# Kernel tuning notes

Measured on AMD Instinct MI355X. Metric: run time of the kernel, lower is better.

The kernel has to match this reference:

```python
import jax, jax.numpy as jnp
import numpy as np

N_NODES = 100000
N_EDGES = 600000
HID = 128
CH_OUT = 3


def setup_inputs() -> dict:
    key = jax.random.key(0)
    ks = jax.random.split(key, 16)
    s = 0.05  # small init to keep tanh in its linear-ish range
    inp = {
        "x": jax.random.normal(ks[0], (N_NODES, HID), dtype=jnp.float32),
        "pos": jax.random.normal(ks[1], (N_NODES, 3), dtype=jnp.float32),
        "edge_index": jax.random.randint(ks[2], (2, N_EDGES), 0, N_NODES, dtype=jnp.int32),
        "fe_w1": jax.random.normal(ks[3], (2 * HID + 1, HID), dtype=jnp.float32) * s,
        "fe_b1": jnp.zeros((HID,), jnp.float32),
        "fe_w2": jax.random.normal(ks[4], (HID, HID), dtype=jnp.float32) * s,
        "fe_b2": jnp.zeros((HID,), jnp.float32),
        "finf_w": jax.random.normal(ks[5], (HID, 1), dtype=jnp.float32) * s,
        "finf_b": jnp.zeros((1,), jnp.float32),
        "fh_w1": jax.random.normal(ks[6], (2 * HID, HID), dtype=jnp.float32) * s,
        "fh_b1": jnp.zeros((HID,), jnp.float32),
        "fh_w2": jax.random.normal(ks[7], (HID, HID), dtype=jnp.float32) * s,
        "fh_b2": jnp.zeros((HID,), jnp.float32),
        "l1_w": jax.random.normal(ks[8], (HID, HID), dtype=jnp.float32) * s,
        "l1_b": jnp.zeros((HID,), jnp.float32),
        "l2_w": jax.random.normal(ks[9], (HID, HID), dtype=jnp.float32) * s,
        "l2_b": jnp.zeros((HID,), jnp.float32),
        "l3_w": jax.random.normal(ks[10], (HID, HID), dtype=jnp.float32) * s,
        "l3_b": jnp.zeros((HID,), jnp.float32),
        "l4_w": jax.random.normal(ks[11], (HID, HID), dtype=jnp.float32) * s,
        "l4_b": jnp.zeros((HID,), jnp.float32),
        "l5_w": jax.random.normal(ks[12], (HID, CH_OUT), dtype=jnp.float32) * s,
        "l5_b": jnp.zeros((CH_OUT,), jnp.float32),
    }
    return inp


def reference(x, pos, edge_index, fe_w1, fe_b1, fe_w2, fe_b2, finf_w, finf_b,
              fh_w1, fh_b1, fh_w2, fh_b2, l1_w, l1_b, l2_w, l2_b, l3_w, l3_b,
              l4_w, l4_b, l5_w, l5_b):
    e_st, e_end = edge_index[0], edge_index[1]
    # dists = ||(pos_i - pos_j)^2||_2  (norm of the squared difference, as in source)
    d = pos[e_st] - pos[e_end]                                  # [E, 3]
    dists = jnp.linalg.norm(jnp.square(d), axis=1, keepdims=True)  # [E, 1]
    # edge MLP f_e
    tmp = jnp.concatenate([x[e_st], x[e_end], dists], axis=1)   # [E, 2H+1]
    m_ij = jnp.tanh(tmp @ fe_w1 + fe_b1)
    m_ij = jnp.tanh(m_ij @ fe_w2 + fe_b2)                        # [E, H]
    # gating f_inf
    e_ij = jnp.tanh(m_ij @ finf_w + finf_b)                      # [E, 1]
    # scatter-sum to source nodes (index_add on edge_index[0])
    m_i = jax.ops.segment_sum(e_ij * m_ij, e_st, num_segments=x.shape[0])  # [N, H]
    # node update f_h with residual
    h = jnp.concatenate([x, m_i], axis=1)                        # [N, 2H]
    x = x + (jnp.tanh(h @ fh_w1 + fh_b1) @ fh_w2 + fh_b2)
    # dense head (dropout p=0.0 is identity)
    lrelu = lambda v: jax.nn.leaky_relu(v, negative_slope=0.01)
    x = lrelu(x @ l1_w + l1_b)
    x = lrelu(x @ l2_w + l2_b)
    x = lrelu(x @ l3_w + l3_b)
    x = lrelu(x @ l4_w + l4_b)
    return x @ l5_w + l5_b
```

## Files before the change

### kernel.cpp

```cpp
#include <hip/hip_runtime.h>
#include <math.h>

#define HID 128

typedef unsigned short u16;
typedef __attribute__((ext_vector_type(8))) short bfrag;
typedef __attribute__((ext_vector_type(4))) float f32x4;
typedef __attribute__((ext_vector_type(8))) unsigned short u16x8;
typedef __attribute__((ext_vector_type(4))) unsigned short u16x4;

__device__ __forceinline__ float fast_tanh(float v) {
    v = fminf(15.0f, fmaxf(-15.0f, v));
    float e = __expf(2.0f * v);
    float r = __builtin_amdgcn_rcpf(e + 1.0f);
    return 1.0f - 2.0f * r;
}

__device__ __forceinline__ u16 f2b(float f) {
    union { float f; unsigned int u; } v;
    v.f = f;
    unsigned int u = v.u;
    return (u16)((u + 0x7FFFu + ((u >> 16) & 1u)) >> 16);
}
__device__ __forceinline__ float b2f(u16 b) {
    union { unsigned int u; float f; } v;
    v.u = ((unsigned int)b) << 16;
    return v.f;
}
__device__ __forceinline__ float bits2f(unsigned u) {
    union { unsigned u; float f; } v; v.u = u; return v.f;
}

__global__ void __launch_bounds__(256) prep_x(const float* __restrict__ x,
                                              u16* __restrict__ xb) {
    int i = blockIdx.x * 256 + threadIdx.x;
    const float4 v0 = *(const float4*)(x + (size_t)i * 8);
    const float4 v1 = *(const float4*)(x + (size_t)i * 8 + 4);
    u16x8 o = { f2b(v0.x), f2b(v0.y), f2b(v0.z), f2b(v0.w),
                f2b(v1.x), f2b(v1.y), f2b(v1.z), f2b(v1.w) };
    *(u16x8*)(xb + (size_t)i * 8) = o;
}

__global__ void __launch_bounds__(256) prep_weights(
    const float* __restrict__ w1, const float* __restrict__ fh1,
    const float* __restrict__ w2, const float* __restrict__ fh2,
    const float* __restrict__ l1, const float* __restrict__ l2,
    const float* __restrict__ l3, const float* __restrict__ l4,
    u16* __restrict__ w1t, u16* __restrict__ fh1t,
    u16* __restrict__ w2t, u16* __restrict__ fh2t,
    u16* __restrict__ l1t, u16* __restrict__ l2t,
    u16* __restrict__ l3t, u16* __restrict__ l4t)
{
    int b = blockIdx.x, t = threadIdx.x;
    const float* src; u16* dst; int K;
    if (b < 256) {
        K = 256;
        if (b < 128) { src = w1;  dst = w1t; }
        else         { src = fh1; dst = fh1t; b -= 128; }
    } else {
        K = 128;
        int s = (b - 256) >> 6; b = (b - 256) & 63;
        switch (s) {
            case 0:  src = w2;  dst = w2t;  break;
            case 1:  src = fh2; dst = fh2t; break;
            case 2:  src = l1;  dst = l1t;  break;
            case 3:  src = l2;  dst = l2t;  break;
            case 4:  src = l3;  dst = l3t;  break;
            default: src = l4;  dst = l4t;  break;
        }
    }
    int idx = b * 256 + t;
    int k = idx >> 7, n = idx & 127;
    dst[(size_t)n * K + k] = f2b(src[(size_t)k * 128 + n]);
}

__global__ void __launch_bounds__(256) hist_kernel(const int* __restrict__ est,
                                                   int* __restrict__ cnt, int E) {
    int e = blockIdx.x * 256 + threadIdx.x;
    if (e < E) atomicAdd(&cnt[est[e]], 1);
}

__global__ void __launch_bounds__(256) scan1(const int* __restrict__ cnt,
                                             int* __restrict__ scanout,
                                             int* __restrict__ partial, int N) {
    __shared__ int s[256];
    int t = threadIdx.x, b = blockIdx.x, i = b * 256 + t;
    int v = (i < N) ? cnt[i] : 0;
    s[t] = v; __syncthreads();
#pragma unroll
    for (int d = 1; d < 256; d <<= 1) {
        int add = (t >= d) ? s[t - d] : 0;
        __syncthreads();
        s[t] += add;
        __syncthreads();
    }
    if (i < N) scanout[i] = s[t] - v;
    if (t == 255) partial[b] = s[255];
}

__global__ void __launch_bounds__(512) scan2(int* __restrict__ partial, int NB) {
    __shared__ int s[512];
    int t = threadIdx.x;
    int v = (t < NB) ? partial[t] : 0;
    s[t] = v; __syncthreads();
#pragma unroll
    for (int d = 1; d < 512; d <<= 1) {
        int add = (t >= d) ? s[t - d] : 0;
        __syncthreads();
        s[t] += add;
        __syncthreads();
    }
    if (t < NB) partial[t] = s[t] - v;
}

__global__ void __launch_bounds__(256) scan3(const int* __restrict__ scanout,
                                             const int* __restrict__ partial,
                                             int* __restrict__ offs,
                                             int* __restrict__ cur, int N, int E) {
    int t = threadIdx.x, b = blockIdx.x, i = b * 256 + t;
    if (i < N) { int o = scanout[i] + partial[b]; offs[i] = o; cur[i] = o; }
    if (i == 0) offs[N] = E;
}

__global__ void __launch_bounds__(256) reorder_kernel(const int* __restrict__ est,
                                                      int* __restrict__ cur,
                                                      int* __restrict__ inv, int E) {
    int e = blockIdx.x * 256 + threadIdx.x;
    if (e < E) { int p = atomicAdd(&cur[est[e]], 1); inv[e] = p; }
}

template<int KD>
__device__ __forceinline__ void gemm_k(const u16* sbuf, const u16* __restrict__ wt,
                                       int w, int l16, int l4g, f32x4 (&acc)[2][2]) {
    const int RS = KD * 2;
#pragma unroll
    for (int k0 = 0; k0 < KD; k0 += 32) {
        const int kb = k0 * 2 + l4g * 16;
        bfrag a0 = *(const bfrag*)((const char*)sbuf +
                    (unsigned)((l16 * RS + kb) ^ ((l16 & 7) << 4)));
        bfrag a1 = *(const bfrag*)((const char*)sbuf +
                    (unsigned)(((16 + l16) * RS + kb) ^ ((l16 & 7) << 4)));
        bfrag b0 = *(const bfrag*)((const char*)wt + (size_t)(32 * w + l16) * RS + kb);
        bfrag b1 = *(const bfrag*)((const char*)wt + (size_t)(32 * w + 16 + l16) * RS + kb);
        acc[0][0] = __builtin_amdgcn_mfma_f32_16x16x32_bf16(a0, b0, acc[0][0], 0, 0, 0);
        acc[0][1] = __builtin_amdgcn_mfma_f32_16x16x32_bf16(a0, b1, acc[0][1], 0, 0, 0);
        acc[1][0] = __builtin_amdgcn_mfma_f32_16x16x32_bf16(a1, b0, acc[1][0], 0, 0, 0);
        acc[1][1] = __builtin_amdgcn_mfma_f32_16x16x32_bf16(a1, b1, acc[1][1], 0, 0, 0);
    }
}

__global__ void __launch_bounds__(256, 2)
egc_edge_csr(const u16* __restrict__ xb, const float* __restrict__ pos,
             const int* __restrict__ est, const int* __restrict__ eend,
             const int* __restrict__ inv,
             const u16* __restrict__ w1t, const float* __restrict__ w1last,
             const float* __restrict__ b1, const u16* __restrict__ w2t,
             const float* __restrict__ b2, u16* __restrict__ g, int n_tiles)
{
    __shared__ __attribute__((aligned(16))) u16 a_sh[2][32 * 256];
    __shared__ __attribute__((aligned(16))) u16 m1_sh[32 * 128];
    __shared__ float dist_l[2][32];
    __shared__ int   dst_l[2][32];

    const int t = threadIdx.x, lane = t & 63, w = t >> 6;
    const int l16 = lane & 15, l4g = lane >> 4;
    const unsigned swz = (unsigned)((l16 & 7) << 4);

    bfrag wa10[8], wa11[8], w2f0[4], w2f1[4];
#pragma unroll
    for (int i = 0; i < 8; ++i) {
        int kb = i * 64 + l4g * 16;
        wa10[i] = *(const bfrag*)((const char*)w1t + (size_t)(32 * w + l16) * 512 + kb);
        wa11[i] = *(const bfrag*)((const char*)w1t + (size_t)(32 * w + 16 + l16) * 512 + kb);
    }
#pragma unroll
    for (int i = 0; i < 4; ++i) {
        int kb = i * 64 + l4g * 16;
        w2f0[i] = *(const bfrag*)((const char*)w2t + (size_t)(32 * w + l16) * 256 + kb);
        w2f1[i] = *(const bfrag*)((const char*)w2t + (size_t)(32 * w + 16 + l16) * 256 + kb);
    }
    float w1l_r[2][4], b1_r[2][4], b2_r[2][4];
#pragma unroll
    for (int mi = 0; mi < 2; ++mi)
#pragma unroll
        for (int rg = 0; rg < 4; ++rg) {
            int n = 32 * w + 16 * mi + l4g * 4 + rg;
            w1l_r[mi][rg] = w1last[n];
            b1_r[mi][rg]  = b1[n];
            b2_r[mi][rg]  = b2[n];
        }

    float4 sv0, sv1, sv2, sv3;
    float pax = 0, pay = 0, paz = 0, pbx = 0, pby = 0, pbz = 0;
    int sdst = 0;

#define EDGE_ISSUE(TILE) do {                                                  \
        int e0_ = (TILE) * 32;                                                 \
        { int f_ = t;       int e_ = f_ >> 5, q_ = f_ & 31; int ge_ = e0_ + e_;\
          int nd_ = (q_ < 16) ? est[ge_] : eend[ge_];                          \
          sv0 = *(const float4*)(xb + (size_t)nd_ * 128 + (q_ & 15) * 8); }    \
        { int f_ = t + 256; int e_ = f_ >> 5, q_ = f_ & 31; int ge_ = e0_ + e_;\
          int nd_ = (q_ < 16) ? est[ge_] : eend[ge_];                          \
          sv1 = *(const float4*)(xb + (size_t)nd_ * 128 + (q_ & 15) * 8); }    \
        { int f_ = t + 512; int e_ = f_ >> 5, q_ = f_ & 31; int ge_ = e0_ + e_;\
          int nd_ = (q_ < 16) ? est[ge_] : eend[ge_];                          \
          sv2 = *(const float4*)(xb + (size_t)nd_ * 128 + (q_ & 15) * 8); }    \
        { int f_ = t + 768; int e_ = f_ >> 5, q_ = f_ & 31; int ge_ = e0_ + e_;\
          int nd_ = (q_ < 16) ? est[ge_] : eend[ge_];                          \
          sv3 = *(const float4*)(xb + (size_t)nd_ * 128 + (q_ & 15) * 8); }    \
        if (t < 32) {                                                          \
            int ge_ = e0_ + t;                                                 \
            int a_ = est[ge_], b_ = eend[ge_];                                 \
            sdst = inv[ge_];                                                   \
            pax = pos[a_ * 3]; pay = pos[a_ * 3 + 1]; paz = pos[a_ * 3 + 2];   \
            pbx = pos[b_ * 3]; pby = pos[b_ * 3 + 1]; pbz = pos[b_ * 3 + 2];   \
        }                                                                      \
    } while (0)

#define EDGE_COMMIT(BUF) do {                                                  \
        { int f_ = t;       int e_ = f_ >> 5, q_ = f_ & 31;                    \
          unsigned by_ = (unsigned)(e_ * 512 + q_ * 16) ^ (unsigned)((e_ & 7) << 4); \
          *(float4*)((char*)a_sh[BUF] + by_) = sv0; }                          \
        { int f_ = t + 256; int e_ = f_ >> 5, q_ = f_ & 31;                    \
          unsigned by_ = (unsigned)(e_ * 512 + q_ * 16) ^ (unsigned)((e_ & 7) << 4); \
          *(float4*)((char*)a_sh[BUF] + by_) = sv1; }                          \
        { int f_ = t + 512; int e_ = f_ >> 5, q_ = f_ & 31;                    \
          unsigned by_ = (unsigned)(e_ * 512 + q_ * 16) ^ (unsigned)((e_ & 7) << 4); \
          *(float4*)((char*)a_sh[BUF] + by_) = sv2; }                          \
        { int f_ = t + 768; int e_ = f_ >> 5, q_ = f_ & 31;                    \
          unsigned by_ = (unsigned)(e_ * 512 + q_ * 16) ^ (unsigned)((e_ & 7) << 4); \
          *(float4*)((char*)a_sh[BUF] + by_) = sv3; }                          \
        if (t < 32) {                                                          \
            float dx_ = pax - pbx, dy_ = pay - pby, dz_ = paz - pbz;           \
            dx_ *= dx_; dy_ *= dy_; dz_ *= dz_;                                \
            dist_l[BUF][t] = sqrtf(dx_ * dx_ + dy_ * dy_ + dz_ * dz_);         \
            dst_l[BUF][t] = sdst;                                              \
        }                                                                      \
    } while (0)

    int tile = blockIdx.x;
    EDGE_ISSUE(tile);
    int buf = 0;

    while (true) {
        EDGE_COMMIT(buf);
        __syncthreads();
        int next = tile + gridDim.x;
        if (next < n_tiles) EDGE_ISSUE(next);

        {
            f32x4 acc[2][2] = {};
#pragma unroll
            for (int i = 0; i < 8; ++i) {
                int kb = i * 64 + l4g * 16;
                bfrag be0 = *(const bfrag*)((const char*)a_sh[buf] +
                            ((unsigned)(l16 * 512 + kb) ^ swz));
                bfrag be1 = *(const bfrag*)((const char*)a_sh[buf] +
                            ((unsigned)((16 + l16) * 512 + kb) ^ swz));
                acc[0][0] = __builtin_amdgcn_mfma_f32_16x16x32_bf16(wa10[i], be0, acc[0][0], 0, 0, 0);
                acc[0][1] = __builtin_amdgcn_mfma_f32_16x16x32_bf16(wa10[i], be1, acc[0][1], 0, 0, 0);
                acc[1][0] = __builtin_amdgcn_mfma_f32_16x16x32_bf16(wa11[i], be0, acc[1][0], 0, 0, 0);
                acc[1][1] = __builtin_amdgcn_mfma_f32_16x16x32_bf16(wa11[i], be1, acc[1][1], 0, 0, 0);
            }
            float de0 = dist_l[buf][l16];
            float de1 = dist_l[buf][16 + l16];
#pragma unroll
            for (int mi = 0; mi < 2; ++mi)
#pragma unroll
                for (int ni = 0; ni < 2; ++ni) {
                    float de = ni ? de1 : de0;
                    u16x4 pk;
#pragma unroll
                    for (int rg = 0; rg < 4; ++rg) {
                        float v = fast_tanh(acc[mi][ni][rg] + de * w1l_r[mi][rg] + b1_r[mi][rg]);
                        pk[rg] = f2b(v);
                    }
                    unsigned byte = ((unsigned)((16 * ni + l16) * 256 +
                                     (32 * w + 16 * mi + l4g * 4) * 2)) ^ swz;
                    *(u16x4*)((char*)m1_sh + byte) = pk;
                }
        }
        __syncthreads();

        {
            f32x4 acc[2][2] = {};
#pragma unroll
            for (int i = 0; i < 4; ++i) {
                int kb = i * 64 + l4g * 16;
                bfrag me0 = *(const bfrag*)((const char*)m1_sh +
                            ((unsigned)(l16 * 256 + kb) ^ swz));
                bfrag me1 = *(const bfrag*)((const char*)m1_sh +
                            ((unsigned)((16 + l16) * 256 + kb) ^ swz));
                acc[0][0] = __builtin_amdgcn_mfma_f32_16x16x32_bf16(w2f0[i], me0, acc[0][0], 0, 0, 0);
                acc[0][1] = __builtin_amdgcn_mfma_f32_16x16x32_bf16(w2f0[i], me1, acc[0][1], 0, 0, 0);
                acc[1][0] = __builtin_amdgcn_mfma_f32_16x16x32_bf16(w2f1[i], me0, acc[1][0], 0, 0, 0);
                acc[1][1] = __builtin_amdgcn_mfma_f32_16x16x32_bf16(w2f1[i], me1, acc[1][1], 0, 0, 0);
            }
            int dr0 = dst_l[buf][l16];
            int dr1 = dst_l[buf][16 + l16];
#pragma unroll
            for (int mi = 0; mi < 2; ++mi)
#pragma unroll
                for (int ni = 0; ni < 2; ++ni) {
                    u16x4 pk;
#pragma unroll
                    for (int rg = 0; rg < 4; ++rg)
                        pk[rg] = f2b(fast_tanh(acc[mi][ni][rg] + b2_r[mi][rg]));
                    int dstrow = ni ? dr1 : dr0;
                    u16* dp = g + (size_t)dstrow * 128 + (32 * w + 16 * mi + l4g * 4);
                    *(u16x4*)dp = pk;
                }
        }

        tile = next; buf ^= 1;
        if (tile >= n_tiles) break;
    }
#undef EDGE_ISSUE
#undef EDGE_COMMIT
}

__global__ void __launch_bounds__(256, 8)
gather_gate(const u16* __restrict__ g, const int* __restrict__ offs,
            const float* __restrict__ fw, const float* __restrict__ fb,
            u16* __restrict__ m_i)
{
    const int lane = threadIdx.x & 63;
    const int n = blockIdx.x * 4 + (threadIdx.x >> 6);
    const float fw0 = fw[2 * lane], fw1 = fw[2 * lane + 1];
    const float fbv = fb[0];
    const int beg = offs[n], end = offs[n + 1];
    const unsigned* g32 = (const unsigned*)g;
    float a0 = 0.0f, a1 = 0.0f;
    int e = beg;
    for (; e + 1 < end; e += 2) {
        unsigned v0 = g32[(size_t)e * 64 + lane];
        unsigned v1 = g32[(size_t)(e + 1) * 64 + lane];
        float f00 = bits2f(v0 << 16), f01 = bits2f(v0 & 0xFFFF0000u);
        float f10 = bits2f(v1 << 16), f11 = bits2f(v1 & 0xFFFF0000u);
        float s0 = f00 * fw0 + f01 * fw1;
        float s1 = f10 * fw0 + f11 * fw1;
#pragma unroll
        for (int m = 1; m < 64; m <<= 1) {
            s0 += __shfl_xor(s0, m);
            s1 += __shfl_xor(s1, m);
        }
        float ev0 = fast_tanh(s0 + fbv);
        float ev1 = fast_tanh(s1 + fbv);
        a0 += ev0 * f00 + ev1 * f10;
        a1 += ev0 * f01 + ev1 * f11;
    }
    if (e < end) {
        unsigned v0 = g32[(size_t)e * 64 + lane];
        float f00 = bits2f(v0 << 16), f01 = bits2f(v0 & 0xFFFF0000u);
        float s0 = f00 * fw0 + f01 * fw1;
#pragma unroll
        for (int m = 1; m < 64; m <<= 1) s0 += __shfl_xor(s0, m);
        float ev0 = fast_tanh(s0 + fbv);
        a0 += ev0 * f00;
        a1 += ev0 * f01;
    }
    unsigned o = (unsigned)f2b(a0) | ((unsigned)f2b(a1) << 16);
    ((unsigned*)m_i)[(size_t)n * 64 + lane] = o;
}

__global__ void __launch_bounds__(256, 3)
egc_edge_mfma(const u16* __restrict__ xb, const float* __restrict__ pos,
              const int* __restrict__ est, const int* __restrict__ eend,
              const u16* __restrict__ w1t, const float* __restrict__ w1last,
              const float* __restrict__ b1, const u16* __restrict__ w2t,
              const float* __restrict__ b2, const float* __restrict__ fw,
              const float* __restrict__ fb, float* __restrict__ m_i)
{
    __shared__ __attribute__((aligned(16))) u16 a_sh[32 * 256];
    __shared__ __attribute__((aligned(16))) u16 m1_sh[32 * 128];
    __shared__ float m2_sh[32][132];
    __shared__ float dist_l[32];
    __shared__ float ev_l[32];
    __shared__ int   st_l[32];

    const int t = threadIdx.x;
    const int e0 = blockIdx.x * 32;
    const int lane = t & 63;
    const int w = t >> 6;
    const int l16 = lane & 15, l4g = lane >> 4;

#pragma unroll
    for (int i = 0; i < 4; ++i) {
        int f = t + 256 * i;
        int e = f >> 5, q = f & 31;
        int ge = e0 + e;
        int node = (q < 16) ? est[ge] : eend[ge];
        float4 v = *(const float4*)(xb + (size_t)node * 128 + (q & 15) * 8);
        unsigned byte = (unsigned)(e * 512 + q * 16) ^ (unsigned)((e & 7) << 4);
        *(float4*)((char*)a_sh + byte) = v;
    }
    if (t < 32) {
        int ge = e0 + t;
        int a = est[ge], b = eend[ge];
        st_l[t] = a;
        float dx = pos[a * 3 + 0] - pos[b * 3 + 0];
        float dy = pos[a * 3 + 1] - pos[b * 3 + 1];
        float dz = pos[a * 3 + 2] - pos[b * 3 + 2];
        dx *= dx; dy *= dy; dz *= dz;
        dist_l[t] = sqrtf(dx * dx + dy * dy + dz * dz);
    }
    __syncthreads();

    {
        f32x4 acc[2][2] = {};
        gemm_k<256>(a_sh, w1t, w, l16, l4g, acc);
#pragma unroll
        for (int mi = 0; mi < 2; ++mi)
#pragma unroll
            for (int ni = 0; ni < 2; ++ni) {
                const int col = 32 * w + 16 * ni + l16;
                const float wl = w1last[col], bb = b1[col];
#pragma unroll
                for (int rg = 0; rg < 4; ++rg) {
                    const int row = 16 * mi + l4g * 4 + rg;
                    float v = fast_tanh(acc[mi][ni][rg] + dist_l[row] * wl + bb);
                    unsigned byte = (unsigned)((row * 256 + col * 2) ^ ((row & 7) << 4));
                    *(u16*)((char*)m1_sh + byte) = f2b(v);
                }
            }
    }
    __syncthreads();

    {
        f32x4 acc[2][2] = {};
        gemm_k<128>(m1_sh, w2t, w, l16, l4g, acc);
#pragma unroll
        for (int mi = 0; mi < 2; ++mi)
#pragma unroll
            for (int ni = 0; ni < 2; ++ni) {
                const int col = 32 * w + 16 * ni + l16;
                const float bb = b2[col];
#pragma unroll
                for (int rg = 0; rg < 4; ++rg) {
                    const int row = 16 * mi + l4g * 4 + rg;
                    m2_sh[row][col] = fast_tanh(acc[mi][ni][rg] + bb);
                }
            }
    }
    __syncthreads();

    if (t < 128) {
        int e = t >> 2, p = t & 3;
        float s = 0.0f;
#pragma unroll
        for (int k = 0; k < 32; ++k) s += m2_sh[e][p * 32 + k] * fw[p * 32 + k];
        s += __shfl_xor(s, 1);
        s += __shfl_xor(s, 2);
        if (p == 0) ev_l[e] = fast_tanh(s + fb[0]);
    }
    __syncthreads();

    {
        int e = t >> 3, l8 = t & 7;
        float ev = ev_l[e];
        size_t base = (size_t)st_l[e] * HID + l8;
#pragma unroll
        for (int i = 0; i < 16; ++i)
            unsafeAtomicAdd(m_i + base + 8 * i, ev * m2_sh[e][l8 + 8 * i]);
    }
}

#define NODE_LAYER(SRC, KD, WT, BIAS, EPILOG)                                  \
    {                                                                          \
        f32x4 acc[2][2] = {};                                                  \
        gemm_k<KD>(SRC, WT, w, l16, l4g, acc);                                 \
        _Pragma("unroll")                                                      \
        for (int mi = 0; mi < 2; ++mi)                                         \
            _Pragma("unroll")                                                  \
            for (int ni = 0; ni < 2; ++ni) {                                   \
                const int col = 32 * w + 16 * ni + l16;                        \
                const float bb = (BIAS)[col];                                  \
                _Pragma("unroll")                                              \
                for (int rg = 0; rg < 4; ++rg) {                               \
                    const int row = 16 * mi + l4g * 4 + rg;                    \
                    float v = acc[mi][ni][rg] + bb;                            \
                    EPILOG;                                                    \
                }                                                              \
            }                                                                  \
    }

#define STORE_BF16(DST) do {                                                   \
        unsigned byte = (unsigned)((row * 256 + col * 2) ^ ((row & 7) << 4));  \
        *(u16*)((char*)(DST) + byte) = f2b(v);                                 \
    } while (0)

template<bool MIBF16>
__global__ void __launch_bounds__(256, 3)
egc_node_mfma(const u16* __restrict__ xb, const float* __restrict__ xf,
              const void* __restrict__ m_i,
              const u16* __restrict__ fh1t, const float* __restrict__ hb1,
              const u16* __restrict__ fh2t, const float* __restrict__ hb2,
              const u16* __restrict__ l1t, const float* __restrict__ l1b,
              const u16* __restrict__ l2t, const float* __restrict__ l2b,
              const u16* __restrict__ l3t, const float* __restrict__ l3b,
              const u16* __restrict__ l4t, const float* __restrict__ l4b,
              const float* __restrict__ l5w, const float* __restrict__ l5b,
              float* __restrict__ out)
{
    __shared__ __attribute__((aligned(16))) u16 a_sh[32 * 256];
    __shared__ __attribute__((aligned(16))) u16 bA[32 * 128];
    __shared__ __attribute__((aligned(16))) u16 bB[32 * 128];
    __shared__ float ff[32][132];

    const int t = threadIdx.x;
    const int n0 = blockIdx.x * 32;
    const int lane = t & 63;
    const int w = t >> 6;
    const int l16 = lane & 15, l4g = lane >> 4;

#pragma unroll
    for (int i = 0; i < 2; ++i) {
        int f = t + 256 * i;
        int n = f >> 4, q = f & 15;
        float4 v = *(const float4*)(xb + (size_t)(n0 + n) * 128 + q * 8);
        unsigned byte = (unsigned)((n * 512 + q * 16) ^ ((n & 7) << 4));
        *(float4*)((char*)a_sh + byte) = v;
    }
    if (MIBF16) {
#pragma unroll
        for (int i = 0; i < 2; ++i) {
            int f = t + 256 * i;
            int n = f >> 4, q = f & 15;
            float4 v = *(const float4*)((const u16*)m_i + (size_t)(n0 + n) * 128 + q * 8);
            unsigned byte = (unsigned)((n * 512 + 256 + q * 16) ^ ((n & 7) << 4));
            *(float4*)((char*)a_sh + byte) = v;
        }
    } else {
#pragma unroll
        for (int i = 0; i < 2; ++i) {
            int f = t + 256 * i;
            int n = f >> 4, q = f & 15;
            const float* src = (const float*)m_i + (size_t)(n0 + n) * 128 + q * 8;
            float4 v0 = *(const float4*)(src);
            float4 v1 = *(const float4*)(src + 4);
            u16x8 o = { f2b(v0.x), f2b(v0.y), f2b(v0.z), f2b(v0.w),
                        f2b(v1.x), f2b(v1.y), f2b(v1.z), f2b(v1.w) };
            unsigned byte = (unsigned)((n * 512 + 256 + q * 16) ^ ((n & 7) << 4));
            *(u16x8*)((char*)a_sh + byte) = o;
        }
    }
    __syncthreads();

    NODE_LAYER(a_sh, 256, fh1t, hb1, { v = fast_tanh(v); STORE_BF16(bA); })
    __syncthreads();
    NODE_LAYER(bA, 128, fh2t, hb2,
               { v += xf[(size_t)(n0 + row) * HID + col]; STORE_BF16(bB); })
    __syncthreads();
    NODE_LAYER(bB, 128, l1t, l1b, { v = v > 0.0f ? v : 0.01f * v; STORE_BF16(bA); })
    __syncthreads();
    NODE_LAYER(bA, 128, l2t, l2b, { v = v > 0.0f ? v : 0.01f * v; STORE_BF16(bB); })
    __syncthreads();
    NODE_LAYER(bB, 128, l3t, l3b, { v = v > 0.0f ? v : 0.01f * v; STORE_BF16(bA); })
    __syncthreads();
    NODE_LAYER(bA, 128, l4t, l4b, { ff[row][col] = v > 0.0f ? v : 0.01f * v; })
    __syncthreads();

    if (t < 96) {
        int n = t / 3, cc = t % 3;
        float s = l5b[cc];
#pragma unroll 8
        for (int k = 0; k < HID; ++k) s += ff[n][k] * l5w[k * 3 + cc];
        out[(size_t)(n0 + n) * 3 + cc] = s;
    }
}

extern "C" void kernel_launch(void* const* d_in, const int* in_sizes, int n_in,
                              void* d_out, int out_size, void* d_ws, size_t ws_size,
                              hipStream_t stream)
{
    const float* x      = (const float*)d_in[0];
    const float* pos    = (const float*)d_in[1];
    const int*   eidx   = (const int*)d_in[2];
    const float* fe_w1  = (const float*)d_in[3];
    const float* fe_b1  = (const float*)d_in[4];
    const float* fe_w2  = (const float*)d_in[5];
    const float* fe_b2  = (const float*)d_in[6];
    const float* finf_w = (const float*)d_in[7];
    const float* finf_b = (const float*)d_in[8];
    const float* fh_w1  = (const float*)d_in[9];
    const float* fh_b1  = (const float*)d_in[10];
    const float* fh_w2  = (const float*)d_in[11];
    const float* fh_b2  = (const float*)d_in[12];
    const float* l1w    = (const float*)d_in[13];
    const float* l1b    = (const float*)d_in[14];
    const float* l2w    = (const float*)d_in[15];
    const float* l2b    = (const float*)d_in[16];
    const float* l3w    = (const float*)d_in[17];
    const float* l3b    = (const float*)d_in[18];
    const float* l4w    = (const float*)d_in[19];
    const float* l4b    = (const float*)d_in[20];
    const float* l5w    = (const float*)d_in[21];
    const float* l5b    = (const float*)d_in[22];
    float* out = (float*)d_out;

    const int n_edges = in_sizes[2] / 2;
    const int n_nodes = in_sizes[0] / HID;
    const int nsb     = (n_nodes + 255) / 256;
    const int n_tiles = n_edges / 32;

    char* ws = (char*)d_ws;
    const bool use_csr = (ws_size >= 208800000ULL);

    if (use_csr) {
        u16* g    = (u16*)(ws + 0);
        u16* xb   = (u16*)(ws + 153600000);
        u16* m_i  = (u16*)(ws + 179200000);
        u16* w1t  = (u16*)(ws + 204800000);
        u16* w2t  = (u16*)(ws + 204865536);
        u16* fh1t = (u16*)(ws + 204898304);
        u16* fh2t = (u16*)(ws + 204963840);
        u16* l1t  = (u16*)(ws + 204996608);
        u16* l2t  = (u16*)(ws + 205029376);
        u16* l3t  = (u16*)(ws + 205062144);
        u16* l4t  = (u16*)(ws + 205094912);
        int* cnt  = (int*)(ws + 205127680);
        int* offs = (int*)(ws + 205527680);
        int* cur  = (int*)(ws + 205927696);
        int* inv  = (int*)(ws + 206327696);
        int* part = (int*)(ws + 208727696);

        (void)hipMemsetAsync(cnt, 0, (size_t)n_nodes * sizeof(int), stream);
        prep_x<<<dim3((n_nodes * HID) / (256 * 8)), dim3(256), 0, stream>>>(x, xb);
        prep_weights<<<dim3(640), dim3(256), 0, stream>>>(
            fe_w1, fh_w1, fe_w2, fh_w2, l1w, l2w, l3w, l4w,
            w1t, fh1t, w2t, fh2t, l1t, l2t, l3t, l4t);

        hist_kernel<<<dim3((n_edges + 255) / 256), dim3(256), 0, stream>>>(eidx, cnt, n_edges);
        scan1<<<dim3(nsb), dim3(256), 0, stream>>>(cnt, cnt, part, n_nodes);
        scan2<<<dim3(1), dim3(512), 0, stream>>>(part, nsb);
        scan3<<<dim3(nsb), dim3(256), 0, stream>>>(cnt, part, offs, cur, n_nodes, n_edges);
        reorder_kernel<<<dim3((n_edges + 255) / 256), dim3(256), 0, stream>>>(eidx, cur, inv, n_edges);

        egc_edge_csr<<<dim3(512), dim3(256), 0, stream>>>(
            xb, pos, eidx, eidx + n_edges, inv, w1t, fe_w1 + (size_t)256 * HID, fe_b1,
            w2t, fe_b2, g, n_tiles);

        gather_gate<<<dim3(n_nodes / 4), dim3(256), 0, stream>>>(g, offs, finf_w, finf_b, m_i);

        egc_node_mfma<true><<<dim3(n_nodes / 32), dim3(256), 0, stream>>>(
            xb, x, m_i, fh1t, fh_b1, fh2t, fh_b2, l1t, l1b, l2t, l2b,
            l3t, l3b, l4t, l4b, l5w, l5b, out);
    } else {
        float* m_i = (float*)(ws + 0);
        u16* xb    = (u16*)(ws + 51200000);
        u16* w1t   = (u16*)(ws + 76800000);
        u16* w2t   = (u16*)(ws + 76865536);
        u16* fh1t  = (u16*)(ws + 76898304);
        u16* fh2t  = (u16*)(ws + 76963840);
        u16* l1t   = (u16*)(ws + 76996608);
        u16* l2t   = (u16*)(ws + 77029376);
        u16* l3t   = (u16*)(ws + 77062144);
        u16* l4t   = (u16*)(ws + 77094912);

        (void)hipMemsetAsync(m_i, 0, (size_t)n_nodes * HID * sizeof(float), stream);
        prep_x<<<dim3((n_nodes * HID) / (256 * 8)), dim3(256), 0, stream>>>(x, xb);
        prep_weights<<<dim3(640), dim3(256), 0, stream>>>(
            fe_w1, fh_w1, fe_w2, fh_w2, l1w, l2w, l3w, l4w,
            w1t, fh1t, w2t, fh2t, l1t, l2t, l3t, l4t);

        egc_edge_mfma<<<dim3(n_edges / 32), dim3(256), 0, stream>>>(
            xb, pos, eidx, eidx + n_edges, w1t, fe_w1 + (size_t)256 * HID, fe_b1,
            w2t, fe_b2, finf_w, finf_b, m_i);

        egc_node_mfma<false><<<dim3(n_nodes / 32), dim3(256), 0, stream>>>(
            xb, x, m_i, fh1t, fh_b1, fh2t, fh_b2, l1t, l1b, l2t, l2b,
            l3t, l3b, l4t, l4b, l5w, l5b, out);
    }
}
```

Before: 384.3 us.

## Sort edges by source, fuse gate into edge kernel, swap node GEMM operands

The reorder kernel now writes sorted source/destination index arrays, so the edge kernel processes edges in CSR order and writes g rows sequentially instead of scattering through an inverse permutation. The f_inf gate dot product and tanh move into the edge kernel epilogue, computed once per edge via a shared-memory reduction. The gather then becomes a plain weighted sum without per-edge wave shuffles. The node kernel swaps the MFMA operands so each lane stores four contiguous channels as vector stores instead of scalar bf16 stores. Occupancy hint and edge grid size also rise. Costs are an extra __syncthreads per tile and est_s/eend_s aliasing the m_i buffer, which is safe only because m_i is written after the edge kernel finishes.

```diff
diff --git a/kernel.cpp b/kernel.cpp
--- a/kernel.cpp
+++ b/kernel.cpp
@@ -123,10 +123,17 @@
 }
 
 __global__ void __launch_bounds__(256) reorder_kernel(const int* __restrict__ est,
+                                                      const int* __restrict__ eend,
                                                       int* __restrict__ cur,
-                                                      int* __restrict__ inv, int E) {
+                                                      int* __restrict__ est_s,
+                                                      int* __restrict__ eend_s, int E) {
     int e = blockIdx.x * 256 + threadIdx.x;
-    if (e < E) { int p = atomicAdd(&cur[est[e]], 1); inv[e] = p; }
+    if (e < E) {
+        int s = est[e];
+        int p = atomicAdd(&cur[s], 1);
+        est_s[p]  = s;
+        eend_s[p] = eend[e];
+    }
 }
 
 template<int KD>
@@ -149,18 +156,39 @@
     }
 }
 
-__global__ void __launch_bounds__(256, 2)
+template<int KD>
+__device__ __forceinline__ void gemm_sw(const u16* act, const u16* __restrict__ wt,
+                                        int w, int l16, int l4g, f32x4 (&acc)[2][2]) {
+    const int RS = KD * 2;
+#pragma unroll
+    for (int k0 = 0; k0 < KD; k0 += 32) {
+        const int kb = k0 * 2 + l4g * 16;
+        bfrag wa0 = *(const bfrag*)((const char*)wt + (size_t)(32 * w + l16) * RS + kb);
+        bfrag wa1 = *(const bfrag*)((const char*)wt + (size_t)(32 * w + 16 + l16) * RS + kb);
+        bfrag be0 = *(const bfrag*)((const char*)act +
+                    (unsigned)((l16 * RS + kb) ^ ((l16 & 7) << 4)));
+        bfrag be1 = *(const bfrag*)((const char*)act +
+                    (unsigned)(((16 + l16) * RS + kb) ^ ((l16 & 7) << 4)));
+        acc[0][0] = __builtin_amdgcn_mfma_f32_16x16x32_bf16(wa0, be0, acc[0][0], 0, 0, 0);
+        acc[0][1] = __builtin_amdgcn_mfma_f32_16x16x32_bf16(wa0, be1, acc[0][1], 0, 0, 0);
+        acc[1][0] = __builtin_amdgcn_mfma_f32_16x16x32_bf16(wa1, be0, acc[1][0], 0, 0, 0);
+        acc[1][1] = __builtin_amdgcn_mfma_f32_16x16x32_bf16(wa1, be1, acc[1][1], 0, 0, 0);
+    }
+}
+
+__global__ void __launch_bounds__(256, 3)
 egc_edge_csr(const u16* __restrict__ xb, const float* __restrict__ pos,
-             const int* __restrict__ est, const int* __restrict__ eend,
-             const int* __restrict__ inv,
+             const int* __restrict__ est_s, const int* __restrict__ eend_s,
              const u16* __restrict__ w1t, const float* __restrict__ w1last,
              const float* __restrict__ b1, const u16* __restrict__ w2t,
-             const float* __restrict__ b2, u16* __restrict__ g, int n_tiles)
+             const float* __restrict__ b2, const float* __restrict__ fw,
+             const float* __restrict__ fb, u16* __restrict__ g,
+             float* __restrict__ ev, int n_tiles)
 {
     __shared__ __attribute__((aligned(16))) u16 a_sh[2][32 * 256];
     __shared__ __attribute__((aligned(16))) u16 m1_sh[32 * 128];
+    __shared__ float red[32][16];
     __shared__ float dist_l[2][32];
-    __shared__ int   dst_l[2][32];
 
     const int t = threadIdx.x, lane = t & 63, w = t >> 6;
     const int l16 = lane & 15, l4g = lane >> 4;
@@ -179,7 +207,7 @@
         w2f0[i] = *(const bfrag*)((const char*)w2t + (size_t)(32 * w + l16) * 256 + kb);
         w2f1[i] = *(const bfrag*)((const char*)w2t + (size_t)(32 * w + 16 + l16) * 256 + kb);
     }
-    float w1l_r[2][4], b1_r[2][4], b2_r[2][4];
+    float w1l_r[2][4], b1_r[2][4], b2_r[2][4], fw_r[2][4];
 #pragma unroll
     for (int mi = 0; mi < 2; ++mi)
 #pragma unroll
@@ -188,30 +216,30 @@
             w1l_r[mi][rg] = w1last[n];
             b1_r[mi][rg]  = b1[n];
             b2_r[mi][rg]  = b2[n];
+            fw_r[mi][rg]  = fw[n];
         }
+    const float fbv = fb[0];
 
     float4 sv0, sv1, sv2, sv3;
     float pax = 0, pay = 0, paz = 0, pbx = 0, pby = 0, pbz = 0;
-    int sdst = 0;
 
 #define EDGE_ISSUE(TILE) do {                                                  \
         int e0_ = (TILE) * 32;                                                 \
         { int f_ = t;       int e_ = f_ >> 5, q_ = f_ & 31; int ge_ = e0_ + e_;\
-          int nd_ = (q_ < 16) ? est[ge_] : eend[ge_];                          \
+          int nd_ = (q_ < 16) ? est_s[ge_] : eend_s[ge_];                      \
           sv0 = *(const float4*)(xb + (size_t)nd_ * 128 + (q_ & 15) * 8); }    \
         { int f_ = t + 256; int e_ = f_ >> 5, q_ = f_ & 31; int ge_ = e0_ + e_;\
-          int nd_ = (q_ < 16) ? est[ge_] : eend[ge_];                          \
+          int nd_ = (q_ < 16) ? est_s[ge_] : eend_s[ge_];                      \
           sv1 = *(const float4*)(xb + (size_t)nd_ * 128 + (q_ & 15) * 8); }    \
         { int f_ = t + 512; int e_ = f_ >> 5, q_ = f_ & 31; int ge_ = e0_ + e_;\
-          int nd_ = (q_ < 16) ? est[ge_] : eend[ge_];                          \
+          int nd_ = (q_ < 16) ? est_s[ge_] : eend_s[ge_];                      \
           sv2 = *(const float4*)(xb + (size_t)nd_ * 128 + (q_ & 15) * 8); }    \
         { int f_ = t + 768; int e_ = f_ >> 5, q_ = f_ & 31; int ge_ = e0_ + e_;\
-          int nd_ = (q_ < 16) ? est[ge_] : eend[ge_];                          \
+          int nd_ = (q_ < 16) ? est_s[ge_] : eend_s[ge_];                      \
           sv3 = *(const float4*)(xb + (size_t)nd_ * 128 + (q_ & 15) * 8); }    \
         if (t < 32) {                                                          \
             int ge_ = e0_ + t;                                                 \
-            int a_ = est[ge_], b_ = eend[ge_];                                 \
-            sdst = inv[ge_];                                                   \
+            int a_ = est_s[ge_], b_ = eend_s[ge_];                             \
             pax = pos[a_ * 3]; pay = pos[a_ * 3 + 1]; paz = pos[a_ * 3 + 2];   \
             pbx = pos[b_ * 3]; pby = pos[b_ * 3 + 1]; pbz = pos[b_ * 3 + 2];   \
         }                                                                      \
@@ -234,7 +262,6 @@
             float dx_ = pax - pbx, dy_ = pay - pby, dz_ = paz - pbz;           \
             dx_ *= dx_; dy_ *= dy_; dz_ *= dz_;                                \
             dist_l[BUF][t] = sqrtf(dx_ * dx_ + dy_ * dy_ + dz_ * dz_);         \
-            dst_l[BUF][t] = sdst;                                              \
         }                                                                      \
     } while (0)
 
@@ -247,6 +274,7 @@
         __syncthreads();
         int next = tile + gridDim.x;
         if (next < n_tiles) EDGE_ISSUE(next);
+        const int e0 = tile * 32;
 
         {
             f32x4 acc[2][2] = {};
@@ -296,20 +324,33 @@
                 acc[1][0] = __builtin_amdgcn_mfma_f32_16x16x32_bf16(w2f1[i], me0, acc[1][0], 0, 0, 0);
                 acc[1][1] = __builtin_amdgcn_mfma_f32_16x16x32_bf16(w2f1[i], me1, acc[1][1], 0, 0, 0);
             }
-            int dr0 = dst_l[buf][l16];
-            int dr1 = dst_l[buf][16 + l16];
+            float part0 = 0.0f, part1 = 0.0f;
 #pragma unroll
             for (int mi = 0; mi < 2; ++mi)
 #pragma unroll
                 for (int ni = 0; ni < 2; ++ni) {
                     u16x4 pk;
-#pragma unroll
-                    for (int rg = 0; rg < 4; ++rg)
-                        pk[rg] = f2b(fast_tanh(acc[mi][ni][rg] + b2_r[mi][rg]));
-                    int dstrow = ni ? dr1 : dr0;
-                    u16* dp = g + (size_t)dstrow * 128 + (32 * w + 16 * mi + l4g * 4);
-                    *(u16x4*)dp = pk;
+                    float ps = 0.0f;
+#pragma unroll
+                    for (int rg = 0; rg < 4; ++rg) {
+                        float v = fast_tanh(acc[mi][ni][rg] + b2_r[mi][rg]);
+                        ps += v * fw_r[mi][rg];
+                        pk[rg] = f2b(v);
+                    }
+                    if (ni) part1 += ps; else part0 += ps;
+                    int dstrow = e0 + 16 * ni + l16;
+                    *(u16x4*)(g + (size_t)dstrow * 128 + (32 * w + 16 * mi + l4g * 4)) = pk;
                 }
+            red[l16][w * 4 + l4g]      = part0;
+            red[16 + l16][w * 4 + l4g] = part1;
+        }
+        __syncthreads();
+
+        if (t < 32) {
+            float s = 0.0f;
+#pragma unroll
+            for (int j = 0; j < 16; ++j) s += red[t][j];
+            ev[e0 + t] = fast_tanh(s + fbv);
         }
 
         tile = next; buf ^= 1;
@@ -320,45 +361,31 @@
 }
 
 __global__ void __launch_bounds__(256, 8)
-gather_gate(const u16* __restrict__ g, const int* __restrict__ offs,
-            const float* __restrict__ fw, const float* __restrict__ fb,
-            u16* __restrict__ m_i)
+gather_seq(const u16* __restrict__ g, const float* __restrict__ ev,
+           const int* __restrict__ offs, u16* __restrict__ m_i)
 {
     const int lane = threadIdx.x & 63;
     const int n = blockIdx.x * 4 + (threadIdx.x >> 6);
-    const float fw0 = fw[2 * lane], fw1 = fw[2 * lane + 1];
-    const float fbv = fb[0];
     const int beg = offs[n], end = offs[n + 1];
     const unsigned* g32 = (const unsigned*)g;
-    float a0 = 0.0f, a1 = 0.0f;
+    float a0 = 0.0f, a1 = 0.0f, b0 = 0.0f, b1 = 0.0f;
     int e = beg;
     for (; e + 1 < end; e += 2) {
         unsigned v0 = g32[(size_t)e * 64 + lane];
         unsigned v1 = g32[(size_t)(e + 1) * 64 + lane];
-        float f00 = bits2f(v0 << 16), f01 = bits2f(v0 & 0xFFFF0000u);
-        float f10 = bits2f(v1 << 16), f11 = bits2f(v1 & 0xFFFF0000u);
-        float s0 = f00 * fw0 + f01 * fw1;
-        float s1 = f10 * fw0 + f11 * fw1;
-#pragma unroll
-        for (int m = 1; m < 64; m <<= 1) {
-            s0 += __shfl_xor(s0, m);
-            s1 += __shfl_xor(s1, m);
-        }
-        float ev0 = fast_tanh(s0 + fbv);
-        float ev1 = fast_tanh(s1 + fbv);
-        a0 += ev0 * f00 + ev1 * f10;
-        a1 += ev0 * f01 + ev1 * f11;
+        float e0 = ev[e], e1 = ev[e + 1];
+        a0 += e0 * bits2f(v0 << 16);
+        a1 += e0 * bits2f(v0 & 0xFFFF0000u);
+        b0 += e1 * bits2f(v1 << 16);
+        b1 += e1 * bits2f(v1 & 0xFFFF0000u);
     }
     if (e < end) {
         unsigned v0 = g32[(size_t)e * 64 + lane];
-        float f00 = bits2f(v0 << 16), f01 = bits2f(v0 & 0xFFFF0000u);
-        float s0 = f00 * fw0 + f01 * fw1;
-#pragma unroll
-        for (int m = 1; m < 64; m <<= 1) s0 += __shfl_xor(s0, m);
-        float ev0 = fast_tanh(s0 + fbv);
-        a0 += ev0 * f00;
-        a1 += ev0 * f01;
-    }
+        float e0 = ev[e];
+        a0 += e0 * bits2f(v0 << 16);
+        a1 += e0 * bits2f(v0 & 0xFFFF0000u);
+    }
+    a0 += b0; a1 += b1;
     unsigned o = (unsigned)f2b(a0) | ((unsigned)f2b(a1) << 16);
     ((unsigned*)m_i)[(size_t)n * 64 + lane] = o;
 }
@@ -465,29 +492,33 @@
     }
 }
 
-#define NODE_LAYER(SRC, KD, WT, BIAS, EPILOG)                                  \
+#define NODE_LAYER_SW(SRC, KD, WT, BIAS, DST, ACT)                             \
     {                                                                          \
         f32x4 acc[2][2] = {};                                                  \
-        gemm_k<KD>(SRC, WT, w, l16, l4g, acc);                                 \
+        gemm_sw<KD>(SRC, WT, w, l16, l4g, acc);                                \
+        float bbr[2][4];                                                       \
+        _Pragma("unroll")                                                      \
+        for (int mi = 0; mi < 2; ++mi)                                         \
+            _Pragma("unroll")                                                  \
+            for (int rg = 0; rg < 4; ++rg)                                     \
+                bbr[mi][rg] = (BIAS)[32 * w + 16 * mi + l4g * 4 + rg];         \
         _Pragma("unroll")                                                      \
         for (int mi = 0; mi < 2; ++mi)                                         \
             _Pragma("unroll")                                                  \
             for (int ni = 0; ni < 2; ++ni) {                                   \
-                const int col = 32 * w + 16 * ni + l16;                        \
-                const float bb = (BIAS)[col];                                  \
+                const int node = 16 * ni + l16;                                \
+                const int ch = 32 * w + 16 * mi + l4g * 4;                     \
+                u16x4 pk;                                                      \
                 _Pragma("unroll")                                              \
                 for (int rg = 0; rg < 4; ++rg) {                               \
-                    const int row = 16 * mi + l4g * 4 + rg;                    \
-                    float v = acc[mi][ni][rg] + bb;                            \
-                    EPILOG;                                                    \
+                    float v = acc[mi][ni][rg] + bbr[mi][rg];                   \
+                    ACT;                                                       \
+                    pk[rg] = f2b(v);                                           \
                 }                                                              \
+                unsigned byte = ((unsigned)(node * 256 + ch * 2)) ^ swz;       \
+                *(u16x4*)((char*)(DST) + byte) = pk;                           \
             }                                                                  \
     }
-
-#define STORE_BF16(DST) do {                                                   \
-        unsigned byte = (unsigned)((row * 256 + col * 2) ^ ((row & 7) << 4));  \
-        *(u16*)((char*)(DST) + byte) = f2b(v);                                 \
-    } while (0)
 
 template<bool MIBF16>
 __global__ void __launch_bounds__(256, 3)
@@ -512,6 +543,7 @@
     const int lane = t & 63;
     const int w = t >> 6;
     const int l16 = lane & 15, l4g = lane >> 4;
+    const unsigned swz = (unsigned)((l16 & 7) << 4);
 
 #pragma unroll
     for (int i = 0; i < 2; ++i) {
@@ -546,18 +578,70 @@
     }
     __syncthreads();
 
-    NODE_LAYER(a_sh, 256, fh1t, hb1, { v = fast_tanh(v); STORE_BF16(bA); })
-    __syncthreads();
-    NODE_LAYER(bA, 128, fh2t, hb2,
-               { v += xf[(size_t)(n0 + row) * HID + col]; STORE_BF16(bB); })
-    __syncthreads();
-    NODE_LAYER(bB, 128, l1t, l1b, { v = v > 0.0f ? v : 0.01f * v; STORE_BF16(bA); })
-    __syncthreads();
-    NODE_LAYER(bA, 128, l2t, l2b, { v = v > 0.0f ? v : 0.01f * v; STORE_BF16(bB); })
-    __syncthreads();
-    NODE_LAYER(bB, 128, l3t, l3b, { v = v > 0.0f ? v : 0.01f * v; STORE_BF16(bA); })
-    __syncthreads();
-    NODE_LAYER(bA, 128, l4t, l4b, { ff[row][col] = v > 0.0f ? v : 0.01f * v; })
+    NODE_LAYER_SW(a_sh, 256, fh1t, hb1, bA, { v = fast_tanh(v); })
+    __syncthreads();
+
+    {
+        f32x4 acc[2][2] = {};
+        gemm_sw<128>(bA, fh2t, w, l16, l4g, acc);
+        float bbr[2][4];
+#pragma unroll
+        for (int mi = 0; mi < 2; ++mi)
+#pragma unroll
+            for (int rg = 0; rg < 4; ++rg)
+                bbr[mi][rg] = hb2[32 * w + 16 * mi + l4g * 4 + rg];
+#pragma unroll
+        for (int mi = 0; mi < 2; ++mi)
+#pragma unroll
+            for (int ni = 0; ni < 2; ++ni) {
+                const int node = 16 * ni + l16;
+                const int ch = 32 * w + 16 * mi + l4g * 4;
+                float4 xr = *(const float4*)(xf + (size_t)(n0 + node) * 128 + ch);
+                u16x4 pk;
+                pk[0] = f2b(acc[mi][ni][0] + bbr[mi][0] + xr.x);
+                pk[1] = f2b(acc[mi][ni][1] + bbr[mi][1] + xr.y);
+                pk[2] = f2b(acc[mi][ni][2] + bbr[mi][2] + xr.z);
+                pk[3] = f2b(acc[mi][ni][3] + bbr[mi][3] + xr.w);
+                unsigned byte = ((unsigned)(node * 256 + ch * 2)) ^ swz;
+                *(u16x4*)((char*)bB + byte) = pk;
+            }
+    }
+    __syncthreads();
+
+    NODE_LAYER_SW(bB, 128, l1t, l1b, bA, { v = v > 0.0f ? v : 0.01f * v; })
+    __syncthreads();
+    NODE_LAYER_SW(bA, 128, l2t, l2b, bB, { v = v > 0.0f ? v : 0.01f * v; })
+    __syncthreads();
+    NODE_LAYER_SW(bB, 128, l3t, l3b, bA, { v = v > 0.0f ? v : 0.01f * v; })
+    __syncthreads();
+
+    {
+        f32x4 acc[2][2] = {};
+        gemm_sw<128>(bA, l4t, w, l16, l4g, acc);
+        float bbr[2][4];
+#pragma unroll
+        for (int mi = 0; mi < 2; ++mi)
+#pragma unroll
+            for (int rg = 0; rg < 4; ++rg)
+                bbr[mi][rg] = l4b[32 * w + 16 * mi + l4g * 4 + rg];
+#pragma unroll
+        for (int mi = 0; mi < 2; ++mi)
+#pragma unroll
+            for (int ni = 0; ni < 2; ++ni) {
+                const int node = 16 * ni + l16;
+                const int ch = 32 * w + 16 * mi + l4g * 4;
+                float4 o;
+                float v0 = acc[mi][ni][0] + bbr[mi][0];
+                float v1 = acc[mi][ni][1] + bbr[mi][1];
+                float v2 = acc[mi][ni][2] + bbr[mi][2];
+                float v3 = acc[mi][ni][3] + bbr[mi][3];
+                o.x = v0 > 0.0f ? v0 : 0.01f * v0;
+                o.y = v1 > 0.0f ? v1 : 0.01f * v1;
+                o.z = v2 > 0.0f ? v2 : 0.01f * v2;
+                o.w = v3 > 0.0f ? v3 : 0.01f * v3;
+                *(float4*)(&ff[node][ch]) = o;
+            }
+    }
     __syncthreads();
 
     if (t < 96) {
@@ -607,9 +691,11 @@
     const bool use_csr = (ws_size >= 208800000ULL);
 
     if (use_csr) {
-        u16* g    = (u16*)(ws + 0);
-        u16* xb   = (u16*)(ws + 153600000);
-        u16* m_i  = (u16*)(ws + 179200000);
+        u16* g     = (u16*)(ws + 0);
+        u16* xb    = (u16*)(ws + 153600000);
+        u16* m_i   = (u16*)(ws + 179200000);
+        int* est_s  = (int*)(ws + 179200000);
+        int* eend_s = (int*)(ws + 181600000);
         u16* w1t  = (u16*)(ws + 204800000);
         u16* w2t  = (u16*)(ws + 204865536);
         u16* fh1t = (u16*)(ws + 204898304);
@@ -621,7 +707,7 @@
         int* cnt  = (int*)(ws + 205127680);
         int* offs = (int*)(ws + 205527680);
         int* cur  = (int*)(ws + 205927696);
-        int* inv  = (int*)(ws + 206327696);
+        float* ev = (float*)(ws + 206327696);
         int* part = (int*)(ws + 208727696);
 
         (void)hipMemsetAsync(cnt, 0, (size_t)n_nodes * sizeof(int), stream);
@@ -634,13 +720,14 @@
         scan1<<<dim3(nsb), dim3(256), 0, stream>>>(cnt, cnt, part, n_nodes);
         scan2<<<dim3(1), dim3(512), 0, stream>>>(part, nsb);
         scan3<<<dim3(nsb), dim3(256), 0, stream>>>(cnt, part, offs, cur, n_nodes, n_edges);
-        reorder_kernel<<<dim3((n_edges + 255) / 256), dim3(256), 0, stream>>>(eidx, cur, inv, n_edges);
-
-        egc_edge_csr<<<dim3(512), dim3(256), 0, stream>>>(
-            xb, pos, eidx, eidx + n_edges, inv, w1t, fe_w1 + (size_t)256 * HID, fe_b1,
-            w2t, fe_b2, g, n_tiles);
-
-        gather_gate<<<dim3(n_nodes / 4), dim3(256), 0, stream>>>(g, offs, finf_w, finf_b, m_i);
+        reorder_kernel<<<dim3((n_edges + 255) / 256), dim3(256), 0, stream>>>(
+            eidx, eidx + n_edges, cur, est_s, eend_s, n_edges);
+
+        egc_edge_csr<<<dim3(768), dim3(256), 0, stream>>>(
+            xb, pos, est_s, eend_s, w1t, fe_w1 + (size_t)256 * HID, fe_b1,
+            w2t, fe_b2, finf_w, finf_b, g, ev, n_tiles);
+
+        gather_seq<<<dim3(n_nodes / 4), dim3(256), 0, stream>>>(g, ev, offs, m_i);
 
         egc_node_mfma<true><<<dim3(n_nodes / 32), dim3(256), 0, stream>>>(
             xb, x, m_i, fh1t, fh_b1, fh2t, fh_b2, l1t, l1b, l2t, l2b,
```

Result: slower. 654.1 us (+70.2%).
